# Optimization experiments

Measured on AMD Instinct MI355X. Metric: run time of the kernel, lower is better.

## Reference

```python
import jax, jax.numpy as jnp
import numpy as np

SIZE_MIN, SIZE_MAX = 10.0, 40.0
CROP = 28


def convert_to_box_list(x):
    # [B, C, W, H] -> [W*H, B, C]
    b, c, w, h = x.shape
    return jnp.transpose(x, (2, 3, 0, 1)).reshape(w * h, b, c)


def invert_convert_to_box_list(x, w, h):
    # [W*H, B, C] -> [B, C, W, H]
    n, b, c = x.shape
    return jnp.transpose(x.reshape(w, h, b, c), (2, 3, 0, 1))


def bilinear_sample(img, x, y):
    # img: [C, W, H]; x, y: pixel coords of shape S -> [C, *S]; zero outside.
    C, W, H = img.shape
    x0 = jnp.floor(x); y0 = jnp.floor(y)
    x1 = x0 + 1.0; y1 = y0 + 1.0
    wx1 = x - x0; wx0 = 1.0 - wx1
    wy1 = y - y0; wy0 = 1.0 - wy1
    def fetch(xi, yi):
        valid = ((xi >= 0) & (xi < W) & (yi >= 0) & (yi < H)).astype(img.dtype)
        xc = jnp.clip(xi, 0, W - 1).astype(jnp.int32)
        yc = jnp.clip(yi, 0, H - 1).astype(jnp.int32)
        return img[:, xc, yc] * valid
    return (fetch(x0, y0) * (wx0 * wy0) + fetch(x1, y0) * (wx1 * wy0)
            + fetch(x0, y1) * (wx0 * wy1) + fetch(x1, y1) * (wx1 * wy1))


def crop(bx, by, bw, bh, big, ws, hs):
    # bx..bh: [k, B]; big: [B, C, W, H] -> [k, B, C, ws, hs]
    u = (jnp.arange(ws) + 0.5) / ws
    v = (jnp.arange(hs) + 0.5) / hs
    xs = bx[..., None] - 0.5 * bw[..., None] + u * bw[..., None] - 0.5  # [k,B,ws]
    ys = by[..., None] - 0.5 * bh[..., None] + v * bh[..., None] - 0.5  # [k,B,hs]
    def one(xr, yr, img):
        X = jnp.broadcast_to(xr[:, None], (ws, hs))
        Y = jnp.broadcast_to(yr[None, :], (ws, hs))
        return bilinear_sample(img, X, Y)
    return jax.vmap(jax.vmap(one, (0, 0, 0)), (0, 0, None))(xs, ys, big)


def uncrop(bx, by, bw, bh, small, Wb, Hb):
    # small: [k, B, C, ws, hs] -> [k, B, C, Wb, Hb] (zero outside each box)
    ws, hs = small.shape[-2], small.shape[-1]
    Xc = jnp.arange(Wb) + 0.5
    Yc = jnp.arange(Hb) + 0.5
    xs = (Xc - (bx[..., None] - 0.5 * bw[..., None])) / bw[..., None] * ws - 0.5
    ys = (Yc - (by[..., None] - 0.5 * bh[..., None])) / bh[..., None] * hs - 0.5
    def one(xr, yr, img):
        X = jnp.broadcast_to(xr[:, None], (Wb, Hb))
        Y = jnp.broadcast_to(yr[None, :], (Wb, Hb))
        return bilinear_sample(img, X, Y)
    return jax.vmap(jax.vmap(one, (0, 0, 0)), (0, 0, 0))(xs, ys, small)


def tmaps_to_bb(tmaps, W_raw, H_raw):
    # tmaps: [B, 4, nw, nh] in (0,1) -> box lists [n_all, B]
    nw, nh = tmaps.shape[-2], tmaps.shape[-1]
    tx, ty, tw, th = tmaps[:, 0], tmaps[:, 1], tmaps[:, 2], tmaps[:, 3]
    ix = jnp.arange(nw, dtype=tmaps.dtype)[:, None]
    iy = jnp.arange(nh, dtype=tmaps.dtype)[None, :]
    bx_map = W_raw * (ix + tx) / nw
    by_map = H_raw * (iy + ty) / nh
    bw_map = SIZE_MIN + (SIZE_MAX - SIZE_MIN) * tw
    bh_map = SIZE_MIN + (SIZE_MAX - SIZE_MIN) * th
    tolist = lambda m: convert_to_box_list(m[:, None]).squeeze(-1)
    return tolist(bx_map), tolist(by_map), tolist(bw_map), tolist(bh_map)


def forward_core(logit_mu, zwhere_mu, zwhere_std, eps_zwhere, eps_zinstance,
                 features, w_zwhere, b_zwhere, w_enc, b_enc, w_dec, b_dec, n_objects_max):
    B, Cf, W_raw, H_raw = features.shape
    nw, nh = logit_mu.shape[-2], logit_mu.shape[-1]

    # zwhere posterior sample + KL vs N(0,1)
    zwhere_sample_map = zwhere_mu + zwhere_std * eps_zwhere
    zwhere_kl_map = 0.5 * (zwhere_mu ** 2 + zwhere_std ** 2) - jnp.log(zwhere_std) - 0.5

    # decode zwhere (1x1 conv) -> sigmoid tmaps -> boxes
    tmaps = jax.nn.sigmoid(jnp.einsum('bzwh,cz->bcwh', zwhere_sample_map, w_zwhere)
                           + b_zwhere[None, :, None, None])
    bx_all, by_all, bw_all, bh_all = tmaps_to_bb(tmaps, W_raw, H_raw)

    area_all = bw_all * bh_all
    area_map = invert_convert_to_box_list(area_all[..., None], nw, nh)

    # c sample = logit map (deterministic relaxation of the DPP/Bernoulli sample)
    c_sample_map = logit_mu
    prob_map = jax.nn.sigmoid(c_sample_map)
    c_all = convert_to_box_list(c_sample_map).squeeze(-1)   # [n_all, B]
    prob_all = convert_to_box_list(prob_map).squeeze(-1)

    # top-k per batch element (indices constant wrt grads)
    k = min(n_objects_max, c_all.shape[0])
    idx = jax.lax.stop_gradient(jax.lax.top_k(c_all.T, k)[1].T)  # [k, B]
    take = lambda t: jnp.take_along_axis(t, idx, axis=0)
    c_few, prob_few = take(c_all), take(prob_all)
    bx_few, by_few, bw_few, bh_few = take(bx_all), take(by_all), take(bw_all), take(bh_all)

    zwhere_sample_all = convert_to_box_list(zwhere_sample_map)  # [n_all, B, Z]
    zwhere_kl_all = convert_to_box_list(zwhere_kl_map)
    idx_z = idx[..., None]
    zwhere_sample_few = jnp.take_along_axis(zwhere_sample_all, idx_z, axis=0)
    zwhere_kl_few = jnp.take_along_axis(zwhere_kl_all, idx_z, axis=0)

    # crop full-res features at the k boxes -> [k, B, Cf, CROP, CROP]
    cropped = crop(bx_few, by_few, bw_few, bh_few, features, CROP, CROP)

    # encoder zinstance (flatten + linear -> mu, std)
    flat = cropped.reshape(k, B, -1)
    enc = jnp.einsum('kbf,df->kbd', flat, w_enc) + b_enc
    dim_z = enc.shape[-1] // 2
    zi_mu = enc[..., :dim_z]
    zi_std = jax.nn.softplus(enc[..., dim_z:]) + 1e-4
    zi_sample = zi_mu + zi_std * eps_zinstance
    zi_kl = 0.5 * (zi_mu ** 2 + zi_std ** 2) - jnp.log(zi_std) - 0.5

    # decoder zinstance (linear -> [k, B, 2, CROP, CROP])
    dec = jnp.einsum('kbz,fz->kbf', zi_sample, w_dec) + b_dec
    raw = dec.reshape(k, B, 2, CROP, CROP)
    small = jnp.concatenate([jax.nn.softplus(raw[..., :1, :, :]),
                             jax.nn.sigmoid(raw[..., 1:, :, :])], axis=-3)

    big_stuff = uncrop(bx_few, by_few, bw_few, bh_few,
                       small * c_few[..., None, None, None], W_raw, H_raw)
    big_weight = big_stuff[..., :1, :, :]
    big_img = big_stuff[..., 1:, :, :]

    # from_weights_to_masks over box dim (dim=-5 of [k,B,1,W,H])
    sum_w = jnp.sum(big_weight, axis=0, keepdims=True)
    big_mask = jnp.tanh(sum_w) * (big_weight / jnp.maximum(sum_w, 1e-6))
    big_mask_non = jnp.tanh(big_weight)

    return (prob_map, area_map, c_few, prob_few, bx_few, by_few, bw_few, bh_few,
            big_mask, big_mask_non, big_img,
            zwhere_sample_few, zwhere_kl_few, zi_sample, zi_kl)


def setup_inputs() -> dict:
    key = jax.random.key(0)
    ks = jax.random.split(key, 9)
    B, NW, NH = 8, 32, 32
    W_RAW = H_RAW = 128
    CF, ZW, ZI, K = 32, 8, 32, 48
    fan_in = CF * CROP * CROP
    return {
        "logit_mu": jax.random.normal(ks[0], (B, 1, NW, NH), jnp.float32),
        "zwhere_mu": 0.5 * jax.random.normal(ks[1], (B, ZW, NW, NH), jnp.float32),
        "zwhere_std": jax.random.uniform(ks[2], (B, ZW, NW, NH), jnp.float32, 0.1, 1.0),
        "eps_zwhere": jax.random.normal(ks[3], (B, ZW, NW, NH), jnp.float32),
        "eps_zinstance": jax.random.normal(ks[4], (K, B, ZI), jnp.float32),
        "features": jax.random.normal(ks[5], (B, CF, W_RAW, H_RAW), jnp.float32),
        "w_zwhere": 0.3 * jax.random.normal(ks[6], (4, ZW), jnp.float32),
        "b_zwhere": jnp.zeros((4,), jnp.float32),
        "w_enc": jax.random.normal(ks[7], (2 * ZI, fan_in), jnp.float32) / np.sqrt(fan_in).astype(np.float32),
        "b_enc": jnp.zeros((2 * ZI,), jnp.float32),
        "w_dec": jax.random.normal(ks[8], (2 * CROP * CROP, ZI), jnp.float32) / np.sqrt(ZI).astype(np.float32),
        "b_dec": jnp.zeros((2 * CROP * CROP,), jnp.float32),
        "n_objects_max": 48,
    }


def reference(logit_mu, zwhere_mu, zwhere_std, eps_zwhere, eps_zinstance, features,
              w_zwhere, b_zwhere, w_enc, b_enc, w_dec, b_dec, n_objects_max):
    return forward_core(logit_mu, zwhere_mu, zwhere_std, eps_zwhere, eps_zinstance,
                        features, w_zwhere, b_zwhere, w_enc, b_enc, w_dec, b_dec,
                        n_objects_max)
```

## Files before the change

kernel.cpp:

```cpp
#include <hip/hip_runtime.h>
#include <math.h>

#define B 8
#define NWD 32
#define NHD 32
#define NBOX 1024
#define ZWD 8
#define ZID 32
#define KOBJ 48
#define CFEAT 32
#define WRAW 128
#define HRAW 128
#define CR 28
#define CR2 784
#define FAN 25088
#define KB 384

#define OFF_PROB   0
#define OFF_AREA   8192
#define OFF_CFEW   16384
#define OFF_PFEW   16768
#define OFF_BXF    17152
#define OFF_BYF    17536
#define OFF_BWF    17920
#define OFF_BHF    18304
#define OFF_BMASK  18688
#define OFF_BMASKN 6310144
#define OFF_BIMG   12601600
#define OFF_ZWS    18893056
#define OFF_ZWK    18896128
#define OFF_ZIS    18899200
#define OFF_ZIK    18911488

#define WS_SMALL 32768

#define FSPLIT 112
#define FPB 224
#define MKB 32
#define KSTR 232

typedef __attribute__((ext_vector_type(8))) short bfrag;
typedef __attribute__((ext_vector_type(4))) float f32x4;

__device__ __forceinline__ float sigm(float x){ return 1.0f/(1.0f+expf(-x)); }
__device__ __forceinline__ float softpl(float x){ return fmaxf(x,0.0f) + log1pf(expf(-fabsf(x))); }
__device__ __forceinline__ float ftanh(float x){
  float t = __expf(2.0f*x);
  return 1.0f - __fdividef(2.0f, t + 1.0f);
}
__device__ __forceinline__ unsigned short f2bf(float f){
  unsigned u = __float_as_uint(f);
  unsigned r = u + 0x7FFFu + ((u >> 16) & 1u);
  return (unsigned short)(r >> 16);
}
__device__ __forceinline__ unsigned okey(float f){
  unsigned b = __float_as_uint(f);
  return b ^ ((b & 0x80000000u) ? 0xFFFFFFFFu : 0x80000000u);
}

__global__ __launch_bounds__(256) void maps_topk_kernel(
    const float* __restrict__ logit, const float* __restrict__ zmu,
    const float* __restrict__ zstd, const float* __restrict__ zeps,
    const float* __restrict__ wz, const float* __restrict__ bz,
    float* __restrict__ out){
  const int b  = blockIdx.x >> 2;
  const int sb = blockIdx.x & 3;
  const int tid = threadIdx.x;
  __shared__ unsigned su[NBOX];
  #pragma unroll
  for (int u = 0; u < 4; u++){
    int j = tid + u*256;
    su[j] = okey(logit[b*NBOX + j]);
  }
  const int n = sb*256 + tid;
  const int w = n >> 5, h = n & 31;
  float acc0=bz[0], acc1=bz[1], acc2=bz[2], acc3=bz[3];
  #pragma unroll
  for(int z=0; z<ZWD; z++){
    int id = ((b*ZWD + z)*NWD + w)*NHD + h;
    float s = zmu[id] + zstd[id]*zeps[id];
    acc0 += s*wz[0*ZWD+z]; acc1 += s*wz[1*ZWD+z];
    acc2 += s*wz[2*ZWD+z]; acc3 += s*wz[3*ZWD+z];
  }
  float tx=sigm(acc0), ty=sigm(acc1), tw=sigm(acc2), th=sigm(acc3);
  float bx = (128.0f*((float)w + tx))/32.0f;
  float by = (128.0f*((float)h + ty))/32.0f;
  float bwv = 10.0f + 30.0f*tw;
  float bhv = 10.0f + 30.0f*th;
  float lg = logit[b*NBOX + n];
  out[OFF_PROB + b*NBOX + n] = sigm(lg);
  out[OFF_AREA + b*NBOX + n] = bwv*bhv;
  __syncthreads();
  const unsigned ui = su[n];
  int rank = 0;
  #pragma unroll 8
  for (int j = 0; j < NBOX; j++){
    unsigned uj = su[j];
    rank += (uj > ui || (uj == ui && j < n)) ? 1 : 0;
  }
  if (rank < KOBJ){
    out[OFF_CFEW + rank*B + b] = lg;
    out[OFF_PFEW + rank*B + b] = sigm(lg);
    out[OFF_BXF  + rank*B + b] = bx;
    out[OFF_BYF  + rank*B + b] = by;
    out[OFF_BWF  + rank*B + b] = bwv;
    out[OFF_BHF  + rank*B + b] = bhv;
    #pragma unroll
    for(int z=0; z<ZWD; z++){
      int id = ((b*ZWD + z)*NWD + w)*NHD + h;
      float mu = zmu[id], sd = zstd[id];
      out[OFF_ZWS + (rank*B+b)*ZWD + z] = mu + sd*zeps[id];
      out[OFF_ZWK + (rank*B+b)*ZWD + z] = 0.5f*(mu*mu + sd*sd) - logf(sd) - 0.5f;
    }
  }
}

__global__ __launch_bounds__(256) void enc_kernel(
    const float* __restrict__ feat, const float* __restrict__ wenc,
    const float* __restrict__ outc, float* __restrict__ part){
  __shared__ __align__(16) unsigned short wl[64*KSTR];
  __shared__ __align__(16) unsigned short cl[MKB*KSTR];
  __shared__ float rAx[MKB], rSx[MKB], rAy[MKB], rSy[MKB];
  const int tid = threadIdx.x;
  const int fs  = blockIdx.x % FSPLIT;
  const int kb0 = (blockIdx.x / FSPLIT) * MKB;
  if (tid < MKB){
    float bx = outc[OFF_BXF + kb0 + tid];
    float by = outc[OFF_BYF + kb0 + tid];
    float bw = outc[OFF_BWF + kb0 + tid];
    float bh = outc[OFF_BHF + kb0 + tid];
    float sx = bw * (1.0f/(float)CR), sy = bh * (1.0f/(float)CR);
    rSx[tid] = sx; rSy[tid] = sy;
    rAx[tid] = bx - 0.5f*bw + 0.5f*sx - 0.5f;
    rAy[tid] = by - 0.5f*bh + 0.5f*sy - 0.5f;
  }
  __syncthreads();
  const int fc0 = fs*FPB;
  #pragma unroll
  for (int u = 0; u < 14; u++){
    int idx = u*256 + tid;
    int dd = idx / 56, q = idx - dd*56;
    float4 w4 = *(const float4*)&wenc[(size_t)dd*FAN + fc0 + q*4];
    unsigned long long pk = (unsigned long long)f2bf(w4.x)
      | ((unsigned long long)f2bf(w4.y) << 16)
      | ((unsigned long long)f2bf(w4.z) << 32)
      | ((unsigned long long)f2bf(w4.w) << 48);
    *(unsigned long long*)&wl[dd*KSTR + q*4] = pk;
  }
  #pragma unroll 4
  for (int u = 0; u < 28; u++){
    int idx = u*256 + tid;
    int rr = idx / FPB, ff = idx - rr*FPB;
    int f = fc0 + ff;
    int c = f / CR2; int p = f - c*CR2;
    int i = p / CR;  int j = p - i*CR;
    int kb = kb0 + rr;
    const float* img = feat + (size_t)((kb & (B-1))*CFEAT + c)*(WRAW*HRAW);
    float x = fmaf((float)i, rSx[rr], rAx[rr]);
    float y = fmaf((float)j, rSy[rr], rAy[rr]);
    float x0f = floorf(x), y0f = floorf(y);
    int x0 = (int)x0f, y0 = (int)y0f;
    float wx1 = x - x0f, wx0 = 1.0f - wx1;
    float wy1 = y - y0f, wy0 = 1.0f - wy1;
    if ((unsigned)x0     >= WRAW) wx0 = 0.f;
    if ((unsigned)(x0+1) >= WRAW) wx1 = 0.f;
    if ((unsigned)y0     >= HRAW) wy0 = 0.f;
    if ((unsigned)(y0+1) >= HRAW) wy1 = 0.f;
    int x0c = min(max(x0,0),WRAW-1), x1c = min(max(x0+1,0),WRAW-1);
    int y0c = min(max(y0,0),HRAW-1), y1c = min(max(y0+1,0),HRAW-1);
    const float* r0p = img + x0c*HRAW;
    const float* r1p = img + x1c*HRAW;
    float v = (r0p[y0c]*wy0 + r0p[y1c]*wy1)*wx0
            + (r1p[y0c]*wy0 + r1p[y1c]*wy1)*wx1;
    cl[rr*KSTR + ff] = f2bf(v);
  }
  __syncthreads();
  const int lane = tid & 63, wv = tid >> 6;
  const int h = wv & 1, g = wv >> 1;
  const int lr = lane & 15, lg = lane >> 4;
  f32x4 acc0 = {0.f,0.f,0.f,0.f}, acc1 = {0.f,0.f,0.f,0.f};
  const unsigned short* arow  = &cl[(h*16 + lr)*KSTR + lg*8];
  const unsigned short* brow0 = &wl[(g*32 + lr)*KSTR + lg*8];
  const unsigned short* brow1 = &wl[(g*32 + 16 + lr)*KSTR + lg*8];
  #pragma unroll
  for (int s = 0; s < 7; s++){
    bfrag a  = *(const bfrag*)(arow  + s*32);
    bfrag b0 = *(const bfrag*)(brow0 + s*32);
    bfrag b1 = *(const bfrag*)(brow1 + s*32);
    acc0 = __builtin_amdgcn_mfma_f32_16x16x32_bf16(a, b0, acc0, 0, 0, 0);
    acc1 = __builtin_amdgcn_mfma_f32_16x16x32_bf16(a, b1, acc1, 0, 0, 0);
  }
  float* dst = part + ((size_t)fs*KB + kb0)*64;
  #pragma unroll
  for (int r = 0; r < 4; r++){
    int row = h*16 + lg*4 + r;
    dst[row*64 + g*32 + lr]      = acc0[r];
    dst[row*64 + g*32 + 16 + lr] = acc1[r];
  }
}

__global__ __launch_bounds__(256) void zi_dec_kernel(
    const float* __restrict__ part, const float* __restrict__ benc,
    const float* __restrict__ ieps, const float* __restrict__ wdec,
    const float* __restrict__ bdec, float* __restrict__ out,
    float* __restrict__ ws){
  int kb = blockIdx.x;
  int d = threadIdx.x & 63, seg = threadIdx.x >> 6;
  float s = 0.f;
  for (int f = seg; f < FSPLIT; f += 4)
    s += part[((size_t)f*KB + kb)*64 + d];
  __shared__ float red[4][64];
  __shared__ float zs[ZID];
  __shared__ float cf_s;
  red[seg][d] = s;
  __syncthreads();
  if (threadIdx.x < ZID){
    int dd = threadIdx.x;
    float mu = benc[dd]     + red[0][dd]     + red[1][dd]     + red[2][dd]     + red[3][dd];
    float pe = benc[ZID+dd] + red[0][ZID+dd] + red[1][ZID+dd] + red[2][ZID+dd] + red[3][ZID+dd];
    float sd = softpl(pe) + 1e-4f;
    float zsv = mu + sd*ieps[kb*ZID + dd];
    out[OFF_ZIS + kb*ZID + dd] = zsv;
    out[OFF_ZIK + kb*ZID + dd] = 0.5f*(mu*mu + sd*sd) - logf(sd) - 0.5f;
    zs[dd] = zsv;
  }
  if (threadIdx.x == 0) cf_s = out[OFF_CFEW + kb];
  __syncthreads();
  float cf = cf_s;
  for (int f = threadIdx.x; f < 2*CR2; f += 256){
    float a = bdec[f];
    #pragma unroll
    for (int q = 0; q < 8; q++){
      float4 w4 = *(const float4*)&wdec[f*ZID + q*4];
      a = fmaf(zs[q*4+0], w4.x, a);
      a = fmaf(zs[q*4+1], w4.y, a);
      a = fmaf(zs[q*4+2], w4.z, a);
      a = fmaf(zs[q*4+3], w4.w, a);
    }
    float v = (f < CR2) ? softpl(a) : sigm(a);
    ws[WS_SMALL + (size_t)kb*(2*CR2) + f] = v*cf;
  }
}

__global__ __launch_bounds__(256) void uncrop_compose_kernel(
    const float* __restrict__ ws, float* __restrict__ out){
  const int t = blockIdx.x*256 + threadIdx.x;
  const int b = t >> 14, p = t & 16383;
  const int X = p >> 7, Y = p & 127;
  __shared__ float sAx[KOBJ], sSx[KOBJ], sAy[KOBJ], sSy[KOBJ];
  if (threadIdx.x < KOBJ){
    int k = threadIdx.x;
    float bx = out[OFF_BXF + k*B + b], bw = out[OFF_BWF + k*B + b];
    float by = out[OFF_BYF + k*B + b], bh = out[OFF_BHF + k*B + b];
    float ix = __fdividef((float)CR, bw), iy = __fdividef((float)CR, bh);
    sSx[k] = ix; sAx[k] = (0.5f*bw - bx)*ix - 0.5f;
    sSy[k] = iy; sAy[k] = (0.5f*bh - by)*iy - 0.5f;
  }
  __syncthreads();
  const float xc = (float)X + 0.5f, yc = (float)Y + 0.5f;
  float wr[KOBJ];
  float sum = 0.f;
  #pragma unroll
  for (int k = 0; k < KOBJ; k++){
    float x = fmaf(xc, sSx[k], sAx[k]);
    float y = fmaf(yc, sSy[k], sAy[k]);
    const float* sm = ws + WS_SMALL + (size_t)(k*B + b)*(2*CR2);
    float x0f = floorf(x), y0f = floorf(y);
    int x0 = (int)x0f, y0 = (int)y0f;
    float wx1 = x - x0f, wx0 = 1.0f - wx1;
    float wy1 = y - y0f, wy0 = 1.0f - wy1;
    if ((unsigned)x0     >= CR) wx0 = 0.f;
    if ((unsigned)(x0+1) >= CR) wx1 = 0.f;
    if ((unsigned)y0     >= CR) wy0 = 0.f;
    if ((unsigned)(y0+1) >= CR) wy1 = 0.f;
    int x0c = min(max(x0,0),CR-1), x1c = min(max(x0+1,0),CR-1);
    int y0c = min(max(y0,0),CR-1), y1c = min(max(y0+1,0),CR-1);
    const float* r0 = sm + x0c*CR;
    const float* r1 = sm + x1c*CR;
    float v0 = (r0[y0c]*wy0 + r0[y1c]*wy1)*wx0 + (r1[y0c]*wy0 + r1[y1c]*wy1)*wx1;
    const float* q0 = r0 + CR2;
    const float* q1 = r1 + CR2;
    float v1 = (q0[y0c]*wy0 + q0[y1c]*wy1)*wx0 + (q1[y0c]*wy0 + q1[y1c]*wy1)*wx1;
    wr[k] = v0; sum += v0;
    out[OFF_BIMG + (size_t)(k*B + b)*16384 + p] = v1;
  }
  float th = ftanh(sum);
  float inv = 1.0f / fmaxf(sum, 1e-6f);
  #pragma unroll
  for (int k = 0; k < KOBJ; k++){
    size_t o = (size_t)(k*B + b)*16384 + p;
    out[OFF_BMASK  + o] = th * (wr[k] * inv);
    out[OFF_BMASKN + o] = ftanh(wr[k]);
  }
}

extern "C" void kernel_launch(void* const* d_in, const int* in_sizes, int n_in,
                              void* d_out, int out_size, void* d_ws, size_t ws_size,
                              hipStream_t stream) {
  (void)in_sizes; (void)n_in; (void)out_size; (void)ws_size;
  const float* logit = (const float*)d_in[0];
  const float* zmu   = (const float*)d_in[1];
  const float* zstd  = (const float*)d_in[2];
  const float* zeps  = (const float*)d_in[3];
  const float* ieps  = (const float*)d_in[4];
  const float* feat  = (const float*)d_in[5];
  const float* wz    = (const float*)d_in[6];
  const float* bz    = (const float*)d_in[7];
  const float* wenc  = (const float*)d_in[8];
  const float* benc  = (const float*)d_in[9];
  const float* wdec  = (const float*)d_in[10];
  const float* bdec  = (const float*)d_in[11];
  float* out = (float*)d_out;
  float* ws  = (float*)d_ws;
  float* part = out + OFF_BMASK;

  maps_topk_kernel    <<<B*4, 256, 0, stream>>>(logit, zmu, zstd, zeps, wz, bz, out);
  enc_kernel          <<<(KB/MKB)*FSPLIT, 256, 0, stream>>>(feat, wenc, out, part);
  zi_dec_kernel       <<<KB, 256, 0, stream>>>(part, benc, ieps, wdec, bdec, out, ws);
  uncrop_compose_kernel<<<(B*WRAW*HRAW)/256, 256, 0, stream>>>(ws, out);
}
```

Before: 100.2 us.

## Restructure crop gather per row, reorder enc blocks, vectorize top-k rank scan

The encoder crop-sampling loop is rewritten so each thread handles one 28-pixel crop row. The x interpolation weights and row offsets are computed once per row, and four bf16 results are packed into 64-bit LDS stores, which removes per-element divisions and index math. The enc block order is swapped so consecutive blocks share the same feature-column slice, which should improve L2 reuse of the encoder weights. The top-k rank loop now reads shared memory as uint4. Each thread's gather now walks along a row, which changes memory coalescing across the wave.

```diff
diff --git a/kernel.cpp b/kernel.cpp
--- a/kernel.cpp
+++ b/kernel.cpp
@@ -37,6 +37,7 @@
 #define FSPLIT 112
 #define FPB 224
 #define MKB 32
+#define NKBG 12
 #define KSTR 232
 
 typedef __attribute__((ext_vector_type(8))) short bfrag;
@@ -66,7 +67,7 @@
   const int b  = blockIdx.x >> 2;
   const int sb = blockIdx.x & 3;
   const int tid = threadIdx.x;
-  __shared__ unsigned su[NBOX];
+  __shared__ __align__(16) unsigned su[NBOX];
   #pragma unroll
   for (int u = 0; u < 4; u++){
     int j = tid + u*256;
@@ -92,11 +93,16 @@
   out[OFF_AREA + b*NBOX + n] = bwv*bhv;
   __syncthreads();
   const unsigned ui = su[n];
+  const uint4* su4 = (const uint4*)su;
   int rank = 0;
-  #pragma unroll 8
-  for (int j = 0; j < NBOX; j++){
-    unsigned uj = su[j];
-    rank += (uj > ui || (uj == ui && j < n)) ? 1 : 0;
+  #pragma unroll 4
+  for (int jq = 0; jq < NBOX/4; jq++){
+    uint4 v = su4[jq];
+    int j = jq*4;
+    rank += (v.x > ui || (v.x == ui && j   < n)) ? 1 : 0;
+    rank += (v.y > ui || (v.y == ui && j+1 < n)) ? 1 : 0;
+    rank += (v.z > ui || (v.z == ui && j+2 < n)) ? 1 : 0;
+    rank += (v.w > ui || (v.w == ui && j+3 < n)) ? 1 : 0;
   }
   if (rank < KOBJ){
     out[OFF_CFEW + rank*B + b] = lg;
@@ -122,8 +128,9 @@
   __shared__ __align__(16) unsigned short cl[MKB*KSTR];
   __shared__ float rAx[MKB], rSx[MKB], rAy[MKB], rSy[MKB];
   const int tid = threadIdx.x;
-  const int fs  = blockIdx.x % FSPLIT;
-  const int kb0 = (blockIdx.x / FSPLIT) * MKB;
+  const int kbg = blockIdx.x % NKBG;
+  const int fs  = blockIdx.x / NKBG;
+  const int kb0 = kbg*MKB;
   if (tid < MKB){
     float bx = outc[OFF_BXF + kb0 + tid];
     float by = outc[OFF_BYF + kb0 + tid];
@@ -147,32 +154,42 @@
       | ((unsigned long long)f2bf(w4.w) << 48);
     *(unsigned long long*)&wl[dd*KSTR + q*4] = pk;
   }
-  #pragma unroll 4
-  for (int u = 0; u < 28; u++){
-    int idx = u*256 + tid;
-    int rr = idx / FPB, ff = idx - rr*FPB;
-    int f = fc0 + ff;
-    int c = f / CR2; int p = f - c*CR2;
-    int i = p / CR;  int j = p - i*CR;
-    int kb = kb0 + rr;
+  {
+    const int rr = tid >> 3, r3 = tid & 7;
+    const int base = fs*8 + r3;
+    const int c = base / 28, i = base - c*28;
+    const int kb = kb0 + rr;
     const float* img = feat + (size_t)((kb & (B-1))*CFEAT + c)*(WRAW*HRAW);
     float x = fmaf((float)i, rSx[rr], rAx[rr]);
-    float y = fmaf((float)j, rSy[rr], rAy[rr]);
-    float x0f = floorf(x), y0f = floorf(y);
-    int x0 = (int)x0f, y0 = (int)y0f;
+    float x0f = floorf(x);
+    int x0 = (int)x0f;
     float wx1 = x - x0f, wx0 = 1.0f - wx1;
-    float wy1 = y - y0f, wy0 = 1.0f - wy1;
     if ((unsigned)x0     >= WRAW) wx0 = 0.f;
     if ((unsigned)(x0+1) >= WRAW) wx1 = 0.f;
-    if ((unsigned)y0     >= HRAW) wy0 = 0.f;
-    if ((unsigned)(y0+1) >= HRAW) wy1 = 0.f;
-    int x0c = min(max(x0,0),WRAW-1), x1c = min(max(x0+1,0),WRAW-1);
-    int y0c = min(max(y0,0),HRAW-1), y1c = min(max(y0+1,0),HRAW-1);
-    const float* r0p = img + x0c*HRAW;
-    const float* r1p = img + x1c*HRAW;
-    float v = (r0p[y0c]*wy0 + r0p[y1c]*wy1)*wx0
-            + (r1p[y0c]*wy0 + r1p[y1c]*wy1)*wx1;
-    cl[rr*KSTR + ff] = f2bf(v);
+    const int xo0 = min(max(x0,0),WRAW-1)*HRAW;
+    const int xo1 = min(max(x0+1,0),WRAW-1)*HRAW;
+    const float Ay = rAy[rr], Sy = rSy[rr];
+    unsigned short* crow = &cl[rr*KSTR + r3*28];
+    #pragma unroll
+    for (int q = 0; q < 28; q += 4){
+      unsigned long long pk = 0ull;
+      #pragma unroll
+      for (int e = 0; e < 4; e++){
+        int j = q + e;
+        float y = fmaf((float)j, Sy, Ay);
+        float y0f = floorf(y);
+        int y0 = (int)y0f;
+        float wy1 = y - y0f, wy0 = 1.0f - wy1;
+        if ((unsigned)y0     >= HRAW) wy0 = 0.f;
+        if ((unsigned)(y0+1) >= HRAW) wy1 = 0.f;
+        int y0c = min(max(y0,0),HRAW-1);
+        int y1c = min(max(y0+1,0),HRAW-1);
+        float v = (img[xo0+y0c]*wy0 + img[xo0+y1c]*wy1)*wx0
+                + (img[xo1+y0c]*wy0 + img[xo1+y1c]*wy1)*wx1;
+        pk |= (unsigned long long)f2bf(v) << (16*e);
+      }
+      *(unsigned long long*)(crow + q) = pk;
+    }
   }
   __syncthreads();
   const int lane = tid & 63, wv = tid >> 6;
@@ -315,7 +332,7 @@
   float* part = out + OFF_BMASK;
 
   maps_topk_kernel    <<<B*4, 256, 0, stream>>>(logit, zmu, zstd, zeps, wz, bz, out);
-  enc_kernel          <<<(KB/MKB)*FSPLIT, 256, 0, stream>>>(feat, wenc, out, part);
+  enc_kernel          <<<NKBG*FSPLIT, 256, 0, stream>>>(feat, wenc, out, part);
   zi_dec_kernel       <<<KB, 256, 0, stream>>>(part, benc, ieps, wdec, bdec, out, ws);
   uncrop_compose_kernel<<<(B*WRAW*HRAW)/256, 256, 0, stream>>>(ws, out);
 }
```

Result: slower. 131.6 us (+31.3%).

## Pre-convert encoder weights to bf16 and read MFMA B fragments from global

Applied to the files above, without the earlier changes.

A new kernel converts the fp32 encoder weight matrix to bf16 once per call into scratch space in the output buffer. The encoder kernel then loads MFMA B fragments straight from that global bf16 copy instead of converting and staging a weight tile in shared memory in every block. This cuts redundant fp32 weight reads and conversion work across the 12 batch-tile blocks that share each feature chunk, and shrinks LDS use. The change also vectorises the top-k rank loop with uint4 LDS reads and unrolls the partial-sum reduction into four accumulators. The cost is an extra kernel launch and an extra global pass over the weights, plus uncoalesced strided global fragment loads in the MFMA loop.

```diff
diff --git a/kernel.cpp b/kernel.cpp
--- a/kernel.cpp
+++ b/kernel.cpp
@@ -34,6 +34,9 @@
 
 #define WS_SMALL 32768
 
+#define SCR_PART 0
+#define SCR_WBF  2752512
+
 #define FSPLIT 112
 #define FPB 224
 #define MKB 32
@@ -56,6 +59,23 @@
 __device__ __forceinline__ unsigned okey(float f){
   unsigned b = __float_as_uint(f);
   return b ^ ((b & 0x80000000u) ? 0xFFFFFFFFu : 0x80000000u);
+}
+
+__global__ __launch_bounds__(256) void wconv_kernel(
+    const float* __restrict__ wenc, unsigned short* __restrict__ wbf){
+  const size_t i0 = ((size_t)blockIdx.x*256 + threadIdx.x)*8;
+  float4 a = *(const float4*)&wenc[i0];
+  float4 b = *(const float4*)&wenc[i0+4];
+  unsigned long long p0 = (unsigned long long)f2bf(a.x)
+    | ((unsigned long long)f2bf(a.y) << 16)
+    | ((unsigned long long)f2bf(a.z) << 32)
+    | ((unsigned long long)f2bf(a.w) << 48);
+  unsigned long long p1 = (unsigned long long)f2bf(b.x)
+    | ((unsigned long long)f2bf(b.y) << 16)
+    | ((unsigned long long)f2bf(b.z) << 32)
+    | ((unsigned long long)f2bf(b.w) << 48);
+  *(unsigned long long*)&wbf[i0]   = p0;
+  *(unsigned long long*)&wbf[i0+4] = p1;
 }
 
 __global__ __launch_bounds__(256) void maps_topk_kernel(
@@ -66,7 +86,7 @@
   const int b  = blockIdx.x >> 2;
   const int sb = blockIdx.x & 3;
   const int tid = threadIdx.x;
-  __shared__ unsigned su[NBOX];
+  __shared__ __align__(16) unsigned su[NBOX];
   #pragma unroll
   for (int u = 0; u < 4; u++){
     int j = tid + u*256;
@@ -92,11 +112,16 @@
   out[OFF_AREA + b*NBOX + n] = bwv*bhv;
   __syncthreads();
   const unsigned ui = su[n];
+  const uint4* su4 = (const uint4*)su;
   int rank = 0;
-  #pragma unroll 8
-  for (int j = 0; j < NBOX; j++){
-    unsigned uj = su[j];
-    rank += (uj > ui || (uj == ui && j < n)) ? 1 : 0;
+  #pragma unroll 4
+  for (int jq = 0; jq < NBOX/4; jq++){
+    uint4 v = su4[jq];
+    int j = jq*4;
+    rank += (v.x > ui || (v.x == ui && j   < n)) ? 1 : 0;
+    rank += (v.y > ui || (v.y == ui && j+1 < n)) ? 1 : 0;
+    rank += (v.z > ui || (v.z == ui && j+2 < n)) ? 1 : 0;
+    rank += (v.w > ui || (v.w == ui && j+3 < n)) ? 1 : 0;
   }
   if (rank < KOBJ){
     out[OFF_CFEW + rank*B + b] = lg;
@@ -116,9 +141,8 @@
 }
 
 __global__ __launch_bounds__(256) void enc_kernel(
-    const float* __restrict__ feat, const float* __restrict__ wenc,
+    const float* __restrict__ feat, const unsigned short* __restrict__ wbf,
     const float* __restrict__ outc, float* __restrict__ part){
-  __shared__ __align__(16) unsigned short wl[64*KSTR];
   __shared__ __align__(16) unsigned short cl[MKB*KSTR];
   __shared__ float rAx[MKB], rSx[MKB], rAy[MKB], rSy[MKB];
   const int tid = threadIdx.x;
@@ -136,17 +160,6 @@
   }
   __syncthreads();
   const int fc0 = fs*FPB;
-  #pragma unroll
-  for (int u = 0; u < 14; u++){
-    int idx = u*256 + tid;
-    int dd = idx / 56, q = idx - dd*56;
-    float4 w4 = *(const float4*)&wenc[(size_t)dd*FAN + fc0 + q*4];
-    unsigned long long pk = (unsigned long long)f2bf(w4.x)
-      | ((unsigned long long)f2bf(w4.y) << 16)
-      | ((unsigned long long)f2bf(w4.z) << 32)
-      | ((unsigned long long)f2bf(w4.w) << 48);
-    *(unsigned long long*)&wl[dd*KSTR + q*4] = pk;
-  }
   #pragma unroll 4
   for (int u = 0; u < 28; u++){
     int idx = u*256 + tid;
@@ -180,13 +193,13 @@
   const int lr = lane & 15, lg = lane >> 4;
   f32x4 acc0 = {0.f,0.f,0.f,0.f}, acc1 = {0.f,0.f,0.f,0.f};
   const unsigned short* arow  = &cl[(h*16 + lr)*KSTR + lg*8];
-  const unsigned short* brow0 = &wl[(g*32 + lr)*KSTR + lg*8];
-  const unsigned short* brow1 = &wl[(g*32 + 16 + lr)*KSTR + lg*8];
+  const unsigned short* bb0 = wbf + (size_t)(g*32 + lr)*FAN + fc0 + lg*8;
+  const unsigned short* bb1 = bb0 + (size_t)16*FAN;
   #pragma unroll
   for (int s = 0; s < 7; s++){
-    bfrag a  = *(const bfrag*)(arow  + s*32);
-    bfrag b0 = *(const bfrag*)(brow0 + s*32);
-    bfrag b1 = *(const bfrag*)(brow1 + s*32);
+    bfrag a  = *(const bfrag*)(arow + s*32);
+    bfrag b0 = *(const bfrag*)(bb0  + s*32);
+    bfrag b1 = *(const bfrag*)(bb1  + s*32);
     acc0 = __builtin_amdgcn_mfma_f32_16x16x32_bf16(a, b0, acc0, 0, 0, 0);
     acc1 = __builtin_amdgcn_mfma_f32_16x16x32_bf16(a, b1, acc1, 0, 0, 0);
   }
@@ -206,13 +219,17 @@
     float* __restrict__ ws){
   int kb = blockIdx.x;
   int d = threadIdx.x & 63, seg = threadIdx.x >> 6;
-  float s = 0.f;
-  for (int f = seg; f < FSPLIT; f += 4)
-    s += part[((size_t)f*KB + kb)*64 + d];
+  float s0=0.f, s1=0.f, s2=0.f, s3=0.f;
+  for (int f = seg; f < FSPLIT; f += 16){
+    s0 += part[((size_t)(f   )*KB + kb)*64 + d];
+    s1 += part[((size_t)(f+ 4)*KB + kb)*64 + d];
+    s2 += part[((size_t)(f+ 8)*KB + kb)*64 + d];
+    s3 += part[((size_t)(f+12)*KB + kb)*64 + d];
+  }
   __shared__ float red[4][64];
   __shared__ float zs[ZID];
   __shared__ float cf_s;
-  red[seg][d] = s;
+  red[seg][d] = (s0+s1) + (s2+s3);
   __syncthreads();
   if (threadIdx.x < ZID){
     int dd = threadIdx.x;
@@ -312,10 +329,13 @@
   const float* bdec  = (const float*)d_in[11];
   float* out = (float*)d_out;
   float* ws  = (float*)d_ws;
-  float* part = out + OFF_BMASK;
-
+  float* scr = out + OFF_BMASK;
+  float* part = scr + SCR_PART;
+  unsigned short* wbf = (unsigned short*)(scr + SCR_WBF);
+
+  wconv_kernel        <<<(FAN*64)/(256*8), 256, 0, stream>>>(wenc, wbf);
   maps_topk_kernel    <<<B*4, 256, 0, stream>>>(logit, zmu, zstd, zeps, wz, bz, out);
-  enc_kernel          <<<(KB/MKB)*FSPLIT, 256, 0, stream>>>(feat, wenc, out, part);
+  enc_kernel          <<<(KB/MKB)*FSPLIT, 256, 0, stream>>>(feat, wbf, out, part);
   zi_dec_kernel       <<<KB, 256, 0, stream>>>(part, benc, ieps, wdec, bdec, out, ws);
   uncrop_compose_kernel<<<(B*WRAW*HRAW)/256, 256, 0, stream>>>(ws, out);
 }
```

Measured after the change: 103.4 us. +3.1%, slower.
